# Performance work log

Measured on AMD Instinct MI355X. Metric: run time of the kernel, lower is better.

Reference implementation:

```python
import jax, jax.numpy as jnp
import numpy as np


def setup_inputs() -> dict:
    key = jax.random.key(0)
    k1, k2 = jax.random.split(key)
    latent = jax.random.normal(k1, (131072, 128), dtype=jnp.float32)
    coords = jax.random.normal(k2, (2048, 128), dtype=jnp.float32)
    return {"latent": latent, "coords": coords}


def reference(latent, coords):
    # torch.cdist(latent, coords).min(1)[1]
    # argmin over euclidean distance == argmin over squared distance,
    # so we skip the sqrt (same result, cheaper and numerically safer).
    x2 = jnp.sum(latent * latent, axis=1, keepdims=True)          # [N, 1]
    c2 = jnp.sum(coords * coords, axis=1)                          # [C]
    cross = latent @ coords.T                                      # [N, C]
    d2 = x2 + c2[None, :] - 2.0 * cross                            # [N, C] squared dists
    return jnp.argmin(d2, axis=1)                                  # [N] int indices
```

## Files before the change

kernel.cpp:

```cpp
#include <hip/hip_runtime.h>


constexpr int D = 128;
constexpr int C = 2048;
constexpr int NCH = 64;
constexpr int NCHUNKS = C / NCH;
constexpr float MARGIN_H = 0.01f;
constexpr int WL_CAP = 32768;

constexpr size_t WS_CNT = 16384;
constexpr size_t WS_WL  = 32768;
constexpr size_t WS_BH  = 262144;
constexpr size_t WS_BL  = 524288;

typedef __attribute__((ext_vector_type(4))) int   i32x4;
typedef unsigned int u32;

__device__ __forceinline__ int pack4(int a0, int a1, int a2, int a3) {
    return (int)(((u32)a0 & 255u) | (((u32)a1 & 255u) << 8) |
                 (((u32)a2 & 255u) << 16) | (((u32)a3 & 255u) << 24));
}

__device__ __forceinline__ void q2(float v, float qa, float inv, float inv128,
                                   int* h, int* l) {
    float hf = __builtin_rintf(v * inv);
    *h = (int)hf;
    float r = fmaf(-hf, qa, v);
    *l = (int)__builtin_rintf(r * inv128);
}

__device__ __forceinline__ void gl_lds16(const void* g, void* l) {
    __builtin_amdgcn_global_load_lds(
        (const __attribute__((address_space(1))) u32*)g,
        (__attribute__((address_space(3))) u32*)l, 16, 0, 0);
}

__global__ void prep_coords(const float* __restrict__ coords,
                            signed char* __restrict__ Bh,
                            signed char* __restrict__ Bl,
                            float2* __restrict__ qc2, int* __restrict__ counter) {
    int t = blockIdx.x * blockDim.x + threadIdx.x;
    if (t == 0) *counter = 0;
    if (t >= C * 4) return;
    int c = t >> 2, p = t & 3;
    float v[32];
#pragma unroll
    for (int i = 0; i < 8; ++i)
        *(float4*)(v + i * 4) = *(const float4*)(coords + (size_t)c * D + p * 32 + i * 4);
    float amax = 0.f, ss = 0.f;
#pragma unroll
    for (int j = 0; j < 32; ++j) {
        amax = fmaxf(amax, fabsf(v[j]));
        ss = fmaf(v[j], v[j], ss);
    }
#pragma unroll
    for (int m = 1; m <= 2; m <<= 1) {
        amax = fmaxf(amax, __shfl_xor(amax, m, 64));
        ss += __shfl_xor(ss, m, 64);
    }
    float qb = fmaxf(amax, 1e-30f) * (1.f / 127.f);
    float inv = 127.f / fmaxf(amax, 1e-30f);
    float inv128 = inv * 128.f;

    int ch = c >> 6, nl = c & 63;
    size_t cbase = (size_t)ch * (NCH * 128) + (size_t)nl * 128;
#pragma unroll
    for (int g = 0; g < 2; ++g) {
        int g8 = p * 2 + g;
        int hw[4], lw[4];
#pragma unroll
        for (int w = 0; w < 4; ++w) {
            int h0, l0, h1, l1, h2, l2, h3, l3;
            q2(v[g * 16 + w * 4 + 0], qb, inv, inv128, &h0, &l0);
            q2(v[g * 16 + w * 4 + 1], qb, inv, inv128, &h1, &l1);
            q2(v[g * 16 + w * 4 + 2], qb, inv, inv128, &h2, &l2);
            q2(v[g * 16 + w * 4 + 3], qb, inv, inv128, &h3, &l3);
            hw[w] = pack4(h0, h1, h2, h3);
            lw[w] = pack4(l0, l1, l2, l3);
        }
        size_t off = cbase + (size_t)(g8 ^ (nl & 7)) * 16;
        *(i32x4*)(Bh + off) = (i32x4){hw[0], hw[1], hw[2], hw[3]};
        *(i32x4*)(Bl + off) = (i32x4){lw[0], lw[1], lw[2], lw[3]};
    }
    if (p == 0) qc2[c] = make_float2(qb, -0.5f * ss);
}


__global__ __launch_bounds__(256, 2) void centroid_fast(
        const float* __restrict__ latent,
        const signed char* __restrict__ Bh_img,
        const signed char* __restrict__ Bl_img,
        const float2* __restrict__ qc2g,
        int* __restrict__ out,
        int* __restrict__ counter,
        int* __restrict__ worklist) {
    __shared__ __align__(16) signed char Bh[2][NCH * 128], Bl[2][NCH * 128];

    const int tid  = threadIdx.x;
    const int wid  = tid >> 6;
    const int lane = tid & 63;
    const int q    = lane >> 4, lr = lane & 15;
    const int row_block = blockIdx.x * 128;

    {
        int ph = (blockIdx.x ^ (blockIdx.x >> 8)) & 3;
        for (int i = 0; i < ph * 2; ++i) __builtin_amdgcn_s_sleep(8);
    }

#pragma unroll
    for (int i = 0; i < 2; ++i) {
        int e = (i * 256 + tid) * 16;
        gl_lds16(Bh_img + e, &Bh[0][e]);
        gl_lds16(Bl_img + e, &Bl[0][e]);
    }

    i32x4 Ah[2][2], Al[2][2];
    float qAr[2][4];
#pragma unroll
    for (int mt = 0; mt < 2; ++mt) {
        const float* rp = latent + (size_t)(row_block + wid * 32 + mt * 16 + lr) * D;
        float v[32];
#pragma unroll
        for (int ks = 0; ks < 2; ++ks)
#pragma unroll
            for (int i = 0; i < 4; ++i)
                *(float4*)(v + ks * 16 + i * 4) =
                    *(const float4*)(rp + ks * 64 + q * 16 + i * 4);
        float amax = 0.f;
#pragma unroll
        for (int j = 0; j < 32; ++j) amax = fmaxf(amax, fabsf(v[j]));
        amax = fmaxf(amax, __shfl_xor(amax, 16, 64));
        amax = fmaxf(amax, __shfl_xor(amax, 32, 64));
        float qa = fmaxf(amax, 1e-30f) * (1.f / 127.f);
        float inv = 127.f / fmaxf(amax, 1e-30f);
        float inv128 = inv * 128.f;
#pragma unroll
        for (int ks = 0; ks < 2; ++ks) {
            int hw[4], lw[4];
#pragma unroll
            for (int w = 0; w < 4; ++w) {
                int h0, l0, h1, l1, h2, l2, h3, l3;
                q2(v[ks * 16 + w * 4 + 0], qa, inv, inv128, &h0, &l0);
                q2(v[ks * 16 + w * 4 + 1], qa, inv, inv128, &h1, &l1);
                q2(v[ks * 16 + w * 4 + 2], qa, inv, inv128, &h2, &l2);
                q2(v[ks * 16 + w * 4 + 3], qa, inv, inv128, &h3, &l3);
                hw[w] = pack4(h0, h1, h2, h3);
                lw[w] = pack4(l0, l1, l2, l3);
            }
            Ah[mt][ks] = (i32x4){hw[0], hw[1], hw[2], hw[3]};
            Al[mt][ks] = (i32x4){lw[0], lw[1], lw[2], lw[3]};
        }
#pragma unroll
        for (int r = 0; r < 4; ++r)
            qAr[mt][r] = __shfl(qa, (lane & 48) | (q * 4 + r), 64);
    }

    float b1[8], b2[8];
    int   bidx[8];
#pragma unroll
    for (int s = 0; s < 8; ++s) { b1[s] = -3.4e38f; b2[s] = -3.4e38f; bidx[s] = 0; }

    __syncthreads();

    for (int ch = 0; ch < NCHUNKS; ++ch) {
        const int buf = ch & 1;
        const int chbase = ch * NCH;
        if (ch + 1 < NCHUNKS) {
            const signed char* sh = Bh_img + (size_t)(ch + 1) * (NCH * 128);
            const signed char* sl = Bl_img + (size_t)(ch + 1) * (NCH * 128);
#pragma unroll
            for (int i = 0; i < 2; ++i) {
                int e = (i * 256 + tid) * 16;
                gl_lds16(sh + e, &Bh[buf ^ 1][e]);
                gl_lds16(sl + e, &Bl[buf ^ 1][e]);
            }
            asm volatile("s_waitcnt vmcnt(4)" ::: "memory");
        } else {
            asm volatile("s_waitcnt vmcnt(0)" ::: "memory");
        }
        __builtin_amdgcn_s_barrier();

        float2 qcv[4];
#pragma unroll
        for (int nt = 0; nt < 4; ++nt) qcv[nt] = qc2g[chbase + nt * 16 + lr];

#pragma unroll
        for (int nt = 0; nt < 4; ++nt) {
            const int nl = nt * 16 + lr;
            i32x4 I1[2], I2[2];
#pragma unroll
            for (int mt = 0; mt < 2; ++mt) {
                I1[mt] = (i32x4){0, 0, 0, 0};
                I2[mt] = (i32x4){0, 0, 0, 0};
            }
            __builtin_amdgcn_s_setprio(1);
#pragma unroll
            for (int ks = 0; ks < 2; ++ks) {
                const int e = nl * 128 + (((ks << 2) | q) ^ (lr & 7)) * 16;
                i32x4 bh = *(const i32x4*)(&Bh[buf][e]);
                i32x4 bl = *(const i32x4*)(&Bl[buf][e]);
#pragma unroll
                for (int mt = 0; mt < 2; ++mt)
                    I1[mt] = __builtin_amdgcn_mfma_i32_16x16x64_i8(Ah[mt][ks], bh, I1[mt], 0, 0, 0);
#pragma unroll
                for (int mt = 0; mt < 2; ++mt)
                    I2[mt] = __builtin_amdgcn_mfma_i32_16x16x64_i8(Ah[mt][ks], bl, I2[mt], 0, 0, 0);
#pragma unroll
                for (int mt = 0; mt < 2; ++mt)
                    I2[mt] = __builtin_amdgcn_mfma_i32_16x16x64_i8(Al[mt][ks], bh, I2[mt], 0, 0, 0);
            }
            __builtin_amdgcn_s_setprio(0);
            const int n_global = chbase + nl;
            const float2 qc = qcv[nt];
#pragma unroll
            for (int mt = 0; mt < 2; ++mt)
#pragma unroll
                for (int r = 0; r < 4; ++r) {
                    int slot = mt * 4 + r;
                    float x = fmaf((float)I2[mt][r], 0.0078125f, (float)I1[mt][r]);
                    float a = fmaf(qAr[mt][r], x * qc.x, qc.y);
                    b2[slot]   = __builtin_amdgcn_fmed3f(a, b1[slot], b2[slot]);
                    bool gt    = a > b1[slot];
                    b1[slot]   = fmaxf(a, b1[slot]);
                    bidx[slot] = gt ? n_global : bidx[slot];
                }
        }
        __builtin_amdgcn_s_barrier();
    }

#pragma unroll
    for (int m = 1; m <= 8; m <<= 1) {
#pragma unroll
        for (int s = 0; s < 8; ++s) {
            float oa = __shfl_xor(b1[s], m, 64);
            float ob = __shfl_xor(b2[s], m, 64);
            int   oi = __shfl_xor(bidx[s], m, 64);
            float mn = fminf(b1[s], oa);
            b2[s] = fmaxf(fmaxf(b2[s], ob), mn);
            bool take = oa > b1[s];
            b1[s]   = take ? oa : b1[s];
            bidx[s] = take ? oi : bidx[s];
        }
    }
#pragma unroll
    for (int s = 0; s < 8; ++s) {
        if (lr == s) {
            int row = row_block + wid * 32 + (s >> 2) * 16 + q * 4 + (s & 3);
            out[row] = bidx[s];
            if (b1[s] - b2[s] < MARGIN_H) {
                int w = atomicAdd(counter, 1);
                if (w < WL_CAP) worklist[w] = row;
            }
        }
    }
}


__global__ __launch_bounds__(1024) void refine_fp64(
        const float* __restrict__ latent, const float* __restrict__ coords,
        const int* __restrict__ worklist, const int* __restrict__ counter,
        int wl_cap, int* __restrict__ out) {
    __shared__ float  xs[D];
    __shared__ double rv[1024];
    __shared__ int    ri[1024];

    int n = *counter;
    if (n > wl_cap) n = wl_cap;

    for (int wi = blockIdx.x; wi < n; wi += gridDim.x) {
        int row = worklist[wi];
        if (threadIdx.x < D)
            xs[threadIdx.x] = latent[(size_t)row * D + threadIdx.x];
        __syncthreads();

        double best = 1.0e300;
        int    bix  = 0;
        for (int c = threadIdx.x; c < C; c += 1024) {
            const float4* cp = (const float4*)(coords + (size_t)c * D);
            double s0 = 0.0, s1 = 0.0, s2 = 0.0, s3 = 0.0;
#pragma unroll 8
            for (int k4 = 0; k4 < 32; ++k4) {
                float4 v = cp[k4];
                double d0 = (double)xs[k4 * 4 + 0] - (double)v.x;
                double d1 = (double)xs[k4 * 4 + 1] - (double)v.y;
                double d2 = (double)xs[k4 * 4 + 2] - (double)v.z;
                double d3 = (double)xs[k4 * 4 + 3] - (double)v.w;
                s0 = fma(d0, d0, s0); s1 = fma(d1, d1, s1);
                s2 = fma(d2, d2, s2); s3 = fma(d3, d3, s3);
            }
            double s = (s0 + s1) + (s2 + s3);
            if (s < best) { best = s; bix = c; }
        }
        rv[threadIdx.x] = best;
        ri[threadIdx.x] = bix;
        __syncthreads();
        for (int off = 512; off > 0; off >>= 1) {
            if (threadIdx.x < off) {
                double ov = rv[threadIdx.x + off];
                int    oi = ri[threadIdx.x + off];
                if (ov < rv[threadIdx.x] ||
                    (ov == rv[threadIdx.x] && oi < ri[threadIdx.x])) {
                    rv[threadIdx.x] = ov;
                    ri[threadIdx.x] = oi;
                }
            }
            __syncthreads();
        }
        if (threadIdx.x == 0) out[row] = ri[0];
        __syncthreads();
    }
}

extern "C" void kernel_launch(void* const* d_in, const int* in_sizes, int n_in,
                              void* d_out, int out_size, void* d_ws, size_t ws_size,
                              hipStream_t stream) {
    const float* latent = (const float*)d_in[0];
    const float* coords = (const float*)d_in[1];
    int*         out    = (int*)d_out;

    char* ws = (char*)d_ws;
    float2* qc2    = (float2*)ws;
    int*    counter = (int*)(ws + WS_CNT);
    int*    wl      = (int*)(ws + WS_WL);
    signed char* Bh = (signed char*)(ws + WS_BH);
    signed char* Bl = (signed char*)(ws + WS_BL);
    const int n_rows = in_sizes[0] / D;

    prep_coords<<<(C * 4) / 256, 256, 0, stream>>>(coords, Bh, Bl, qc2, counter);
    centroid_fast<<<n_rows / 128, 256, 0, stream>>>(latent, Bh, Bl, qc2, out,
                                                    counter, wl);
    refine_fp64<<<608, 1024, 0, stream>>>(latent, coords, wl, counter, WL_CAP, out);
}
```

Baseline: 276.3 us.

## Use global per-tensor scales and pure-integer score tracking in centroid argmin

Switches coordinate quantization from per-row to a single global scale, and uses one per-wave scale for latent rows. The centroid norm term folds into the integer accumulator init, so the per-element epilogue becomes integer shift-add and max/min with no float conversions or per-row scale multiplies. The chunk size is halved to 32 centroids, which cuts LDS per buffer and prefetch per step. Coarser shared scales lose some precision, so the integer margin threshold may send more rows to the fp64 refine pass.

```diff
diff --git a/kernel.cpp b/kernel.cpp
--- a/kernel.cpp
+++ b/kernel.cpp
@@ -3,17 +3,17 @@
 
 constexpr int D = 128;
 constexpr int C = 2048;
-constexpr int NCH = 64;
+constexpr int NCH = 32;
 constexpr int NCHUNKS = C / NCH;
-constexpr float MARGIN_H = 0.01f;
 constexpr int WL_CAP = 32768;
 
 constexpr size_t WS_CNT = 16384;
 constexpr size_t WS_WL  = 32768;
+constexpr size_t WS_C2F = 196608;
 constexpr size_t WS_BH  = 262144;
 constexpr size_t WS_BL  = 524288;
 
-typedef __attribute__((ext_vector_type(4))) int   i32x4;
+typedef __attribute__((ext_vector_type(4))) int i32x4;
 typedef unsigned int u32;
 
 __device__ __forceinline__ int pack4(int a0, int a1, int a2, int a3) {
@@ -35,35 +35,46 @@
         (__attribute__((address_space(3))) u32*)l, 16, 0, 0);
 }
 
-__global__ void prep_coords(const float* __restrict__ coords,
-                            signed char* __restrict__ Bh,
-                            signed char* __restrict__ Bl,
-                            float2* __restrict__ qc2, int* __restrict__ counter) {
+__global__ __launch_bounds__(1024) void prep_coords(
+        const float* __restrict__ coords,
+        signed char* __restrict__ Bh,
+        signed char* __restrict__ Bl,
+        float* __restrict__ c2f, float* __restrict__ qBout,
+        int* __restrict__ counter) {
+    __shared__ float sW[16];
     int t = blockIdx.x * blockDim.x + threadIdx.x;
     if (t == 0) *counter = 0;
-    if (t >= C * 4) return;
+
+    float m = 0.f;
+    for (int i = threadIdx.x; i < C * D / 4; i += 1024) {
+        float4 v = ((const float4*)coords)[i];
+        m = fmaxf(m, fmaxf(fmaxf(fabsf(v.x), fabsf(v.y)),
+                           fmaxf(fabsf(v.z), fabsf(v.w))));
+    }
+#pragma unroll
+    for (int s = 1; s <= 32; s <<= 1) m = fmaxf(m, __shfl_xor(m, s, 64));
+    if ((threadIdx.x & 63) == 0) sW[threadIdx.x >> 6] = m;
+    __syncthreads();
+    float aB = 1e-30f;
+#pragma unroll
+    for (int i = 0; i < 16; ++i) aB = fmaxf(aB, sW[i]);
+
+    float qb = aB * (1.f / 127.f);
+    float inv = 127.f / aB;
+    float inv128 = inv * 128.f;
+    if (t == 0) *qBout = qb;
+
     int c = t >> 2, p = t & 3;
     float v[32];
 #pragma unroll
     for (int i = 0; i < 8; ++i)
         *(float4*)(v + i * 4) = *(const float4*)(coords + (size_t)c * D + p * 32 + i * 4);
-    float amax = 0.f, ss = 0.f;
-#pragma unroll
-    for (int j = 0; j < 32; ++j) {
-        amax = fmaxf(amax, fabsf(v[j]));
-        ss = fmaf(v[j], v[j], ss);
-    }
-#pragma unroll
-    for (int m = 1; m <= 2; m <<= 1) {
-        amax = fmaxf(amax, __shfl_xor(amax, m, 64));
-        ss += __shfl_xor(ss, m, 64);
-    }
-    float qb = fmaxf(amax, 1e-30f) * (1.f / 127.f);
-    float inv = 127.f / fmaxf(amax, 1e-30f);
-    float inv128 = inv * 128.f;
-
-    int ch = c >> 6, nl = c & 63;
-    size_t cbase = (size_t)ch * (NCH * 128) + (size_t)nl * 128;
+    float ss = 0.f;
+#pragma unroll
+    for (int j = 0; j < 32; ++j) ss = fmaf(v[j], v[j], ss);
+#pragma unroll
+    for (int s = 1; s <= 2; s <<= 1) ss += __shfl_xor(ss, s, 64);
+
 #pragma unroll
     for (int g = 0; g < 2; ++g) {
         int g8 = p * 2 + g;
@@ -78,11 +89,11 @@
             hw[w] = pack4(h0, h1, h2, h3);
             lw[w] = pack4(l0, l1, l2, l3);
         }
-        size_t off = cbase + (size_t)(g8 ^ (nl & 7)) * 16;
+        size_t off = (size_t)c * 128 + (size_t)((g8 ^ (c & 7)) * 16);
         *(i32x4*)(Bh + off) = (i32x4){hw[0], hw[1], hw[2], hw[3]};
         *(i32x4*)(Bl + off) = (i32x4){lw[0], lw[1], lw[2], lw[3]};
     }
-    if (p == 0) qc2[c] = make_float2(qb, -0.5f * ss);
+    if (p == 0) c2f[c] = -64.f * ss / qb;
 }
 
 
@@ -90,7 +101,8 @@
         const float* __restrict__ latent,
         const signed char* __restrict__ Bh_img,
         const signed char* __restrict__ Bl_img,
-        const float2* __restrict__ qc2g,
+        const float* __restrict__ c2f,
+        const float* __restrict__ qBp,
         int* __restrict__ out,
         int* __restrict__ counter,
         int* __restrict__ worklist) {
@@ -107,58 +119,63 @@
         for (int i = 0; i < ph * 2; ++i) __builtin_amdgcn_s_sleep(8);
     }
 
-#pragma unroll
-    for (int i = 0; i < 2; ++i) {
-        int e = (i * 256 + tid) * 16;
-        gl_lds16(Bh_img + e, &Bh[0][e]);
-        gl_lds16(Bl_img + e, &Bl[0][e]);
-    }
+    gl_lds16(Bh_img + tid * 16, &Bh[0][tid * 16]);
+    gl_lds16(Bl_img + tid * 16, &Bl[0][tid * 16]);
+
+    const float qB = *qBp;
 
     i32x4 Ah[2][2], Al[2][2];
-    float qAr[2][4];
-#pragma unroll
-    for (int mt = 0; mt < 2; ++mt) {
-        const float* rp = latent + (size_t)(row_block + wid * 32 + mt * 16 + lr) * D;
-        float v[32];
-#pragma unroll
-        for (int ks = 0; ks < 2; ++ks)
-#pragma unroll
-            for (int i = 0; i < 4; ++i)
-                *(float4*)(v + ks * 16 + i * 4) =
-                    *(const float4*)(rp + ks * 64 + q * 16 + i * 4);
+    float invqA, qa;
+    {
+        float v[2][32];
+#pragma unroll
+        for (int mt = 0; mt < 2; ++mt) {
+            const float* rp = latent + (size_t)(row_block + wid * 32 + mt * 16 + lr) * D;
+#pragma unroll
+            for (int ks = 0; ks < 2; ++ks)
+#pragma unroll
+                for (int i = 0; i < 4; ++i)
+                    *(float4*)(v[mt] + ks * 16 + i * 4) =
+                        *(const float4*)(rp + ks * 64 + q * 16 + i * 4);
+        }
         float amax = 0.f;
 #pragma unroll
-        for (int j = 0; j < 32; ++j) amax = fmaxf(amax, fabsf(v[j]));
-        amax = fmaxf(amax, __shfl_xor(amax, 16, 64));
-        amax = fmaxf(amax, __shfl_xor(amax, 32, 64));
-        float qa = fmaxf(amax, 1e-30f) * (1.f / 127.f);
-        float inv = 127.f / fmaxf(amax, 1e-30f);
+        for (int mt = 0; mt < 2; ++mt)
+#pragma unroll
+            for (int j = 0; j < 32; ++j) amax = fmaxf(amax, fabsf(v[mt][j]));
+#pragma unroll
+        for (int s = 1; s <= 32; s <<= 1) amax = fmaxf(amax, __shfl_xor(amax, s, 64));
+        amax = fmaxf(amax, 1e-30f);
+        qa = amax * (1.f / 127.f);
+        invqA = 1.f / qa;
+        float inv = 127.f / amax;
         float inv128 = inv * 128.f;
 #pragma unroll
-        for (int ks = 0; ks < 2; ++ks) {
-            int hw[4], lw[4];
-#pragma unroll
-            for (int w = 0; w < 4; ++w) {
-                int h0, l0, h1, l1, h2, l2, h3, l3;
-                q2(v[ks * 16 + w * 4 + 0], qa, inv, inv128, &h0, &l0);
-                q2(v[ks * 16 + w * 4 + 1], qa, inv, inv128, &h1, &l1);
-                q2(v[ks * 16 + w * 4 + 2], qa, inv, inv128, &h2, &l2);
-                q2(v[ks * 16 + w * 4 + 3], qa, inv, inv128, &h3, &l3);
-                hw[w] = pack4(h0, h1, h2, h3);
-                lw[w] = pack4(l0, l1, l2, l3);
-            }
-            Ah[mt][ks] = (i32x4){hw[0], hw[1], hw[2], hw[3]};
-            Al[mt][ks] = (i32x4){lw[0], lw[1], lw[2], lw[3]};
-        }
-#pragma unroll
-        for (int r = 0; r < 4; ++r)
-            qAr[mt][r] = __shfl(qa, (lane & 48) | (q * 4 + r), 64);
-    }
-
-    float b1[8], b2[8];
-    int   bidx[8];
-#pragma unroll
-    for (int s = 0; s < 8; ++s) { b1[s] = -3.4e38f; b2[s] = -3.4e38f; bidx[s] = 0; }
+        for (int mt = 0; mt < 2; ++mt)
+#pragma unroll
+            for (int ks = 0; ks < 2; ++ks) {
+                int hw[4], lw[4];
+#pragma unroll
+                for (int w = 0; w < 4; ++w) {
+                    int h0, l0, h1, l1, h2, l2, h3, l3;
+                    q2(v[mt][ks * 16 + w * 4 + 0], qa, inv, inv128, &h0, &l0);
+                    q2(v[mt][ks * 16 + w * 4 + 1], qa, inv, inv128, &h1, &l1);
+                    q2(v[mt][ks * 16 + w * 4 + 2], qa, inv, inv128, &h2, &l2);
+                    q2(v[mt][ks * 16 + w * 4 + 3], qa, inv, inv128, &h3, &l3);
+                    hw[w] = pack4(h0, h1, h2, h3);
+                    lw[w] = pack4(l0, l1, l2, l3);
+                }
+                Ah[mt][ks] = (i32x4){hw[0], hw[1], hw[2], hw[3]};
+                Al[mt][ks] = (i32x4){lw[0], lw[1], lw[2], lw[3]};
+            }
+    }
+    const int M_int = (int)(1.28f / (qa * qB)) + 1;
+
+    int b1[8], b2[8], bidx[8];
+#pragma unroll
+    for (int s = 0; s < 8; ++s) {
+        b1[s] = -2147483647 - 1; b2[s] = -2147483647 - 1; bidx[s] = 0;
+    }
 
     __syncthreads();
 
@@ -168,30 +185,27 @@
         if (ch + 1 < NCHUNKS) {
             const signed char* sh = Bh_img + (size_t)(ch + 1) * (NCH * 128);
             const signed char* sl = Bl_img + (size_t)(ch + 1) * (NCH * 128);
-#pragma unroll
-            for (int i = 0; i < 2; ++i) {
-                int e = (i * 256 + tid) * 16;
-                gl_lds16(sh + e, &Bh[buf ^ 1][e]);
-                gl_lds16(sl + e, &Bl[buf ^ 1][e]);
-            }
-            asm volatile("s_waitcnt vmcnt(4)" ::: "memory");
+            gl_lds16(sh + tid * 16, &Bh[buf ^ 1][tid * 16]);
+            gl_lds16(sl + tid * 16, &Bl[buf ^ 1][tid * 16]);
+            asm volatile("s_waitcnt vmcnt(2)" ::: "memory");
         } else {
             asm volatile("s_waitcnt vmcnt(0)" ::: "memory");
         }
         __builtin_amdgcn_s_barrier();
 
-        float2 qcv[4];
-#pragma unroll
-        for (int nt = 0; nt < 4; ++nt) qcv[nt] = qc2g[chbase + nt * 16 + lr];
-
-#pragma unroll
-        for (int nt = 0; nt < 4; ++nt) {
+        float cf[2];
+        cf[0] = c2f[chbase + lr];
+        cf[1] = c2f[chbase + 16 + lr];
+
+#pragma unroll
+        for (int nt = 0; nt < 2; ++nt) {
             const int nl = nt * 16 + lr;
+            const int v0 = (int)__builtin_rintf(cf[nt] * invqA);
             i32x4 I1[2], I2[2];
 #pragma unroll
             for (int mt = 0; mt < 2; ++mt) {
                 I1[mt] = (i32x4){0, 0, 0, 0};
-                I2[mt] = (i32x4){0, 0, 0, 0};
+                I2[mt] = (i32x4){v0, v0, v0, v0};
             }
             __builtin_amdgcn_s_setprio(1);
 #pragma unroll
@@ -211,17 +225,15 @@
             }
             __builtin_amdgcn_s_setprio(0);
             const int n_global = chbase + nl;
-            const float2 qc = qcv[nt];
 #pragma unroll
             for (int mt = 0; mt < 2; ++mt)
 #pragma unroll
                 for (int r = 0; r < 4; ++r) {
                     int slot = mt * 4 + r;
-                    float x = fmaf((float)I2[mt][r], 0.0078125f, (float)I1[mt][r]);
-                    float a = fmaf(qAr[mt][r], x * qc.x, qc.y);
-                    b2[slot]   = __builtin_amdgcn_fmed3f(a, b1[slot], b2[slot]);
-                    bool gt    = a > b1[slot];
-                    b1[slot]   = fmaxf(a, b1[slot]);
+                    int S = (int)(((u32)I1[mt][r] << 7) + (u32)I2[mt][r]);
+                    bool gt  = S > b1[slot];
+                    b2[slot]   = max(b2[slot], min(S, b1[slot]));
+                    b1[slot]   = max(S, b1[slot]);
                     bidx[slot] = gt ? n_global : bidx[slot];
                 }
         }
@@ -232,11 +244,11 @@
     for (int m = 1; m <= 8; m <<= 1) {
 #pragma unroll
         for (int s = 0; s < 8; ++s) {
-            float oa = __shfl_xor(b1[s], m, 64);
-            float ob = __shfl_xor(b2[s], m, 64);
-            int   oi = __shfl_xor(bidx[s], m, 64);
-            float mn = fminf(b1[s], oa);
-            b2[s] = fmaxf(fmaxf(b2[s], ob), mn);
+            int oa = __shfl_xor(b1[s], m, 64);
+            int ob = __shfl_xor(b2[s], m, 64);
+            int oi = __shfl_xor(bidx[s], m, 64);
+            int mn = min(b1[s], oa);
+            b2[s] = max(max(b2[s], ob), mn);
             bool take = oa > b1[s];
             b1[s]   = take ? oa : b1[s];
             bidx[s] = take ? oi : bidx[s];
@@ -247,7 +259,7 @@
         if (lr == s) {
             int row = row_block + wid * 32 + (s >> 2) * 16 + q * 4 + (s & 3);
             out[row] = bidx[s];
-            if (b1[s] - b2[s] < MARGIN_H) {
+            if (b1[s] - b2[s] < M_int) {
                 int w = atomicAdd(counter, 1);
                 if (w < WL_CAP) worklist[w] = row;
             }
@@ -319,15 +331,16 @@
     int*         out    = (int*)d_out;
 
     char* ws = (char*)d_ws;
-    float2* qc2    = (float2*)ws;
+    float*  qB      = (float*)ws;
     int*    counter = (int*)(ws + WS_CNT);
     int*    wl      = (int*)(ws + WS_WL);
+    float*  c2f     = (float*)(ws + WS_C2F);
     signed char* Bh = (signed char*)(ws + WS_BH);
     signed char* Bl = (signed char*)(ws + WS_BL);
     const int n_rows = in_sizes[0] / D;
 
-    prep_coords<<<(C * 4) / 256, 256, 0, stream>>>(coords, Bh, Bl, qc2, counter);
-    centroid_fast<<<n_rows / 128, 256, 0, stream>>>(latent, Bh, Bl, qc2, out,
+    prep_coords<<<8, 1024, 0, stream>>>(coords, Bh, Bl, c2f, qB, counter);
+    centroid_fast<<<n_rows / 128, 256, 0, stream>>>(latent, Bh, Bl, c2f, qB, out,
                                                     counter, wl);
     refine_fp64<<<608, 1024, 0, stream>>>(latent, coords, wl, counter, WL_CAP, out);
 }
```

After: 272.4 us. Within noise of the previous version (-1.4%).
